# Kernel tuning notes

Measured on AMD Instinct MI355X. Metric: run time of the kernel, lower is better.

The kernel has to match this reference:

```python
import jax, jax.numpy as jnp
import numpy as np

V, D, C, B, S, H = 50000, 256, 10, 64, 512, 512


def setup_inputs() -> dict:
    key = jax.random.key(0)
    ks = jax.random.split(key, 12)
    s = 0.02
    return {
        "x": jax.random.randint(ks[0], (B, S), 0, V),
        "embed_w": jax.random.normal(ks[1], (V, D), dtype=jnp.float32) * s,
        "Wl": jax.random.normal(ks[2], (D, D), dtype=jnp.float32) * s,
        "bl": jnp.zeros((D,), jnp.float32),
        "Wsl": jax.random.normal(ks[3], (D, D), dtype=jnp.float32) * s,
        "bsl": jnp.zeros((D,), jnp.float32),
        "Wr": jax.random.normal(ks[4], (D, D), dtype=jnp.float32) * s,
        "br": jnp.zeros((D,), jnp.float32),
        "Wsr": jax.random.normal(ks[5], (D, D), dtype=jnp.float32) * s,
        "bsr": jnp.zeros((D,), jnp.float32),
        "conv_w": jax.random.normal(ks[6], (H, 3 * D), dtype=jnp.float32) * s,
        "conv_b": jnp.zeros((H,), jnp.float32),
        "fc_w": jax.random.normal(ks[7], (C, H), dtype=jnp.float32) * s,
        "fc_b": jnp.zeros((C,), jnp.float32),
        "cl0": jax.random.normal(ks[8], (B, D), dtype=jnp.float32),
        "cr0": jax.random.normal(ks[9], (B, D), dtype=jnp.float32),
    }


def reference(x, embed_w, Wl, bl, Wsl, bsl, Wr, br, Wsr, bsr,
              conv_w, conv_b, fc_w, fc_b, cl0, cr0):
    e = embed_w[x]  # [B,S,D] embedding lookup
    # Precompute the embedding-dependent half of each recurrence (one big GEMM)
    pre_l = jnp.swapaxes(jnp.einsum("bsd,ed->bse", e, Wsl) + bsl, 0, 1)  # [S,B,D]
    pre_r = jnp.swapaxes(jnp.einsum("bsd,ed->bse", e, Wsr) + bsr, 0, 1)  # [S,B,D]

    # left[0]=cl0; left[t]=relu(Wl left[t-1] + Wsl e[t-1])  (output carry, then update)
    def lstep(c, p):
        return jax.nn.relu(c @ Wl.T + bl + p), c

    _, left = jax.lax.scan(lstep, cl0, pre_l)  # [S,B,D]

    # right[S-1]=cr0; right[t]=relu(Wr right[t+1] + Wsr e[t+1])
    def rstep(c, p):
        return jax.nn.relu(c @ Wr.T + br + p), c

    _, right = jax.lax.scan(rstep, cr0, pre_r, reverse=True)  # [S,B,D]

    ctx = jnp.concatenate(
        [jnp.swapaxes(left, 0, 1), e, jnp.swapaxes(right, 0, 1)], axis=-1
    )  # [B,S,3D]
    # Conv2d(1,512,(1,3D)) == per-timestep linear 3D->512
    h = jax.nn.relu(jnp.einsum("bsd,hd->bsh", ctx, conv_w) + conv_b)  # [B,S,H]
    pooled = h.max(axis=1)  # max_pool1d over full sequence -> [B,H]
    return pooled @ fc_w.T + fc_b  # [B,C]
```

## Files before the change

### kernel.cpp

```cpp
#include <hip/hip_runtime.h>
#include <hip/hip_bf16.h>

#define VOCAB 50000
#define DD 256
#define NCLS 10
#define BB 64
#define SS 512
#define HH 512
#define K3D 768

typedef __attribute__((ext_vector_type(8))) short bf16x8;
typedef __attribute__((ext_vector_type(8))) unsigned short ush8;
typedef __attribute__((ext_vector_type(4))) float f32x4;

static __device__ __forceinline__ unsigned short f2bf(float f) {
    __hip_bfloat16 h = __float2bfloat16(f);
    return *reinterpret_cast<unsigned short*>(&h);
}

__global__ __launch_bounds__(256) void prep_gather_kernel(
    const float* __restrict__ conv_w,
    const float* __restrict__ Wsl, const float* __restrict__ Wsr,
    const float* __restrict__ bsl, const float* __restrict__ bl,
    const float* __restrict__ bsr, const float* __restrict__ br,
    const int* __restrict__ x, const float* __restrict__ embed_w,
    unsigned short* __restrict__ convwb,
    unsigned short* __restrict__ wscat,
    float* __restrict__ biascat,
    unsigned short* __restrict__ e2)
{
    const int bid = blockIdx.x;
    if (bid < 192) {
        const int g = bid * 256 + threadIdx.x;
        const float* src = conv_w + (size_t)g * 8;
        const float4 v0 = *(const float4*)(src);
        const float4 v1 = *(const float4*)(src + 4);
        ush8 o;
        o[0]=f2bf(v0.x); o[1]=f2bf(v0.y); o[2]=f2bf(v0.z); o[3]=f2bf(v0.w);
        o[4]=f2bf(v1.x); o[5]=f2bf(v1.y); o[6]=f2bf(v1.z); o[7]=f2bf(v1.w);
        *(ush8*)(convwb + (size_t)g * 8) = o;
    } else if (bid < 256) {
        const int g = (bid - 192) * 256 + threadIdx.x;
        const int row = g >> 5, d0 = (g & 31) * 8;
        const float* src = (row < 256 ? Wsl + (size_t)row * DD
                                      : Wsr + (size_t)(row - 256) * DD) + d0;
        const float4 v0 = *(const float4*)(src);
        const float4 v1 = *(const float4*)(src + 4);
        ush8 o;
        o[0]=f2bf(v0.x); o[1]=f2bf(v0.y); o[2]=f2bf(v0.z); o[3]=f2bf(v0.w);
        o[4]=f2bf(v1.x); o[5]=f2bf(v1.y); o[6]=f2bf(v1.z); o[7]=f2bf(v1.w);
        *(ush8*)(wscat + (size_t)g * 8) = o;
    } else if (bid == 256) {
        for (int i = threadIdx.x; i < 512; i += 256)
            biascat[i] = (i < 256) ? (bsl[i] + bl[i]) : (bsr[i - 256] + br[i - 256]);
    } else {
        const int g = (bid - 257) * 256 + threadIdx.x;
        const int bs = g >> 5;
        const int b = bs >> 9, s = bs & (SS - 1);
        const int d0 = (g & 31) * 8;
        const float* src = embed_w + (size_t)x[bs] * DD + d0;
        const float4 v0 = *(const float4*)(src);
        const float4 v1 = *(const float4*)(src + 4);
        ush8 o;
        o[0]=f2bf(v0.x); o[1]=f2bf(v0.y); o[2]=f2bf(v0.z); o[3]=f2bf(v0.w);
        o[4]=f2bf(v1.x); o[5]=f2bf(v1.y); o[6]=f2bf(v1.z); o[7]=f2bf(v1.w);
        *(ush8*)(e2 + ((size_t)s * BB + b) * DD + d0) = o;
    }
}

#define PPAD 72

__global__ __launch_bounds__(256) void pre_mfma_kernel(
    const unsigned short* __restrict__ wscat,
    const unsigned short* __restrict__ e2,
    const float* __restrict__ biascat,
    float* __restrict__ pre2_l, float* __restrict__ pre2_r)
{
    __shared__ unsigned short Abuf[2][128][PPAD];
    __shared__ unsigned short Bbuf[2][128][PPAD];

    const int mi  = blockIdx.x & 3;
    const int sbi = blockIdx.x >> 2;
    const int tid = threadIdx.x;
    const int w = tid >> 6, lane = tid & 63;
    const int lr = lane & 15, g = lane >> 4;
    const int lk = g * 8;

    f32x4 acc[2][8];
#pragma unroll
    for (int mt = 0; mt < 2; ++mt)
#pragma unroll
        for (int nt = 0; nt < 8; ++nt) acc[mt][nt] = (f32x4)(0.f);

    const int strow = tid >> 3;
    const int skc   = (tid & 7) * 8;

    auto stage = [&](int ks, int buf) {
        const int k0 = ks * 64;
#pragma unroll
        for (int j = 0; j < 4; ++j) {
            const int row = strow + 32 * j;
            *(bf16x8*)&Abuf[buf][row][skc] =
                *(const bf16x8*)(wscat + (size_t)(mi * 128 + row) * DD + k0 + skc);
            *(bf16x8*)&Bbuf[buf][row][skc] =
                *(const bf16x8*)(e2 + (size_t)(sbi * 128 + row) * DD + k0 + skc);
        }
    };

    stage(0, 0);
    int cur = 0;
    for (int ks = 0; ks < 4; ++ks) {
        __syncthreads();
        if (ks + 1 < 4) stage(ks + 1, cur ^ 1);
#pragma unroll
        for (int k2 = 0; k2 < 2; ++k2) {
            const int kk = k2 * 32 + lk;
            const bf16x8 a0 = *(const bf16x8*)&Abuf[cur][w * 32 + lr][kk];
            const bf16x8 a1 = *(const bf16x8*)&Abuf[cur][w * 32 + 16 + lr][kk];
#pragma unroll
            for (int nt = 0; nt < 8; ++nt) {
                const bf16x8 bv = *(const bf16x8*)&Bbuf[cur][nt * 16 + lr][kk];
                acc[0][nt] = __builtin_amdgcn_mfma_f32_16x16x32_bf16(a0, bv, acc[0][nt], 0, 0, 0);
                acc[1][nt] = __builtin_amdgcn_mfma_f32_16x16x32_bf16(a1, bv, acc[1][nt], 0, 0, 0);
            }
        }
        cur ^= 1;
    }

#pragma unroll
    for (int mt = 0; mt < 2; ++mt) {
        const int eg = mi * 128 + w * 32 + mt * 16 + g * 4;
        const float4 bia = *(const float4*)(biascat + eg);
        float* dstb = (eg >= 256) ? pre2_r : pre2_l;
        const int e = eg & 255;
#pragma unroll
        for (int nt = 0; nt < 8; ++nt) {
            const int sb = sbi * 128 + nt * 16 + lr;
            const int s = sb >> 6, bgq = (sb >> 4) & 3, b_loc = sb & 15;
            float4 v;
            v.x = acc[mt][nt][0] + bia.x;
            v.y = acc[mt][nt][1] + bia.y;
            v.z = acc[mt][nt][2] + bia.z;
            v.w = acc[mt][nt][3] + bia.w;
            *(float4*)(dstb + ((size_t)s * 4 + bgq) * 4096 + (e >> 2) * 64 + b_loc * 4) = v;
        }
    }
}

#define CSWZ(row, off) ((off) ^ (((row) & 15) << 4))
#define APAD 72

__global__ __launch_bounds__(256, 1) void recur_conve_kernel(
    const float* __restrict__ Wl, const float* __restrict__ Wr,
    const float* __restrict__ cl0, const float* __restrict__ cr0,
    const float* __restrict__ pre2_l, const float* __restrict__ pre2_r,
    unsigned short* __restrict__ outl, unsigned short* __restrict__ outr,
    const unsigned short* __restrict__ e2,
    const unsigned short* __restrict__ convwb,
    unsigned short* __restrict__ hpart)
{
    __shared__ alignas(16) unsigned char smem[2 * 2 * 128 * APAD * 2];

    const int tid  = threadIdx.x;
    const int lane = tid & 63;

    if (blockIdx.x < 8) {
        unsigned short* cbf0 = (unsigned short*)smem;
        unsigned short* cbf1 = (unsigned short*)smem + 16 * 256;

        const int dir = blockIdx.x >> 2;
        const int bg  = blockIdx.x & 3;
        const int b0  = bg * 16;
        const int wl  = tid >> 6;
        const int col = lane & 15;
        const int g   = lane >> 4;

        const float* W   = dir ? Wr : Wl;
        const float* c0  = dir ? cr0 : cl0;
        const float* pre = dir ? pre2_r : pre2_l;
        unsigned short* out = dir ? outr : outl;

        bf16x8 wfrag[4][8];
#pragma unroll
        for (int mt = 0; mt < 4; ++mt)
#pragma unroll
            for (int i = 0; i < 8; ++i) {
                const int kt = (i + 2 * wl) & 7;
                const float* src = W + (size_t)(wl * 64 + mt * 16 + col) * DD
                                     + kt * 32 + g * 8;
                const float4 lo = *(const float4*)(src);
                const float4 hi = *(const float4*)(src + 4);
                ush8 p;
                p[0]=f2bf(lo.x); p[1]=f2bf(lo.y); p[2]=f2bf(lo.z); p[3]=f2bf(lo.w);
                p[4]=f2bf(hi.x); p[5]=f2bf(hi.y); p[6]=f2bf(hi.z); p[7]=f2bf(hi.w);
                wfrag[mt][i] = *(bf16x8*)&p;
            }

        int soff[8];
#pragma unroll
        for (int i = 0; i < 8; ++i) {
            const int kt = (i + 2 * wl) & 7;
            soff[i] = CSWZ(col, kt * 64 + g * 16);
        }

        {
            const int blc = tid >> 4;
            const int ch  = tid & 15;
            const float* src = c0 + (size_t)(b0 + blc) * DD + ch * 16;
            const float4 v0 = *(const float4*)(src);
            const float4 v1 = *(const float4*)(src + 4);
            const float4 v2 = *(const float4*)(src + 8);
            const float4 v3 = *(const float4*)(src + 12);
            ush8 p0, p1;
            p0[0]=f2bf(v0.x); p0[1]=f2bf(v0.y); p0[2]=f2bf(v0.z); p0[3]=f2bf(v0.w);
            p0[4]=f2bf(v1.x); p0[5]=f2bf(v1.y); p0[6]=f2bf(v1.z); p0[7]=f2bf(v1.w);
            p1[0]=f2bf(v2.x); p1[1]=f2bf(v2.y); p1[2]=f2bf(v2.z); p1[3]=f2bf(v2.w);
            p1[4]=f2bf(v3.x); p1[5]=f2bf(v3.y); p1[6]=f2bf(v3.z); p1[7]=f2bf(v3.w);
            char* rowp = (char*)cbf0 + blc * 512;
            *(ush8*)(rowp + CSWZ(blc, ch * 32))      = p0;
            *(ush8*)(rowp + CSWZ(blc, ch * 32 + 16)) = p1;
            const int t0 = dir ? 511 : 0;
            ush8* dst = (ush8*)(out + ((size_t)t0 * BB + b0 + blc) * DD + ch * 16);
            dst[0] = p0; dst[1] = p1;
        }

        const int lpre = (wl * 16 + g) * 64 + col * 4;
        const ptrdiff_t pstep = dir ? -(ptrdiff_t)16384 : (ptrdiff_t)16384;
        const float* p0 = pre + ((size_t)(dir ? 511 : 0) * 4 + bg) * 4096 + lpre;

        float4 pA0 = *(const float4*)(p0);
        float4 pA1 = *(const float4*)(p0 + 256);
        float4 pA2 = *(const float4*)(p0 + 512);
        float4 pA3 = *(const float4*)(p0 + 768);
        const float* p1p = p0 + pstep;
        float4 pB0 = *(const float4*)(p1p);
        float4 pB1 = *(const float4*)(p1p + 256);
        float4 pB2 = *(const float4*)(p1p + 512);
        float4 pB3 = *(const float4*)(p1p + 768);
        const float* pfetch = p0 + 2 * pstep;

        unsigned short* oplane = out + (size_t)(dir ? 510 : 1) * BB * DD
                                     + (b0 + col) * DD + wl * 64 + g * 4;
        const ptrdiff_t ostep = (dir ? -(ptrdiff_t)1 : (ptrdiff_t)1) * (BB * DD);

        __syncthreads();

        int cur = 0;
#pragma unroll 2
        for (int k = 0; k < SS - 1; ++k) {
            bf16x8 sfrag[8];
            {
                const char* rowp = (const char*)(cur ? cbf1 : cbf0) + col * 512;
#pragma unroll
                for (int i = 0; i < 8; ++i)
                    sfrag[i] = *(const bf16x8*)(rowp + soff[i]);
            }

            const float4 pN0 = *(const float4*)(pfetch);
            const float4 pN1 = *(const float4*)(pfetch + 256);
            const float4 pN2 = *(const float4*)(pfetch + 512);
            const float4 pN3 = *(const float4*)(pfetch + 768);
            if (k < SS - 4) pfetch += pstep;

            char* nbuf = (char*)(cur ? cbf0 : cbf1) + col * 512;

            auto epi = [&](int mt, const f32x4 a) {
                const float v0 = fmaxf(a[0], 0.f);
                const float v1 = fmaxf(a[1], 0.f);
                const float v2 = fmaxf(a[2], 0.f);
                const float v3 = fmaxf(a[3], 0.f);
                uint2 uu;
                asm("v_cvt_pk_bf16_f32 %0, %1, %2" : "=v"(uu.x) : "v"(v0), "v"(v1));
                asm("v_cvt_pk_bf16_f32 %0, %1, %2" : "=v"(uu.y) : "v"(v2), "v"(v3));
                const int eoff = (wl * 64 + mt * 16 + g * 4) * 2;
                *(uint2*)(nbuf + CSWZ(col, eoff)) = uu;
                *(uint2*)(oplane + mt * 16) = uu;
            };

            f32x4 a0 = *(const f32x4*)&pA0;
            f32x4 a1 = *(const f32x4*)&pA1;
            __builtin_amdgcn_s_setprio(1);
#pragma unroll
            for (int i = 0; i < 8; ++i) {
                a0 = __builtin_amdgcn_mfma_f32_16x16x32_bf16(wfrag[0][i], sfrag[i], a0, 0, 0, 0);
                a1 = __builtin_amdgcn_mfma_f32_16x16x32_bf16(wfrag[1][i], sfrag[i], a1, 0, 0, 0);
            }
            __builtin_amdgcn_s_setprio(0);
            epi(0, a0);
            epi(1, a1);

            f32x4 a2 = *(const f32x4*)&pA2;
            f32x4 a3 = *(const f32x4*)&pA3;
            __builtin_amdgcn_s_setprio(1);
#pragma unroll
            for (int i = 0; i < 8; ++i) {
                a2 = __builtin_amdgcn_mfma_f32_16x16x32_bf16(wfrag[2][i], sfrag[i], a2, 0, 0, 0);
                a3 = __builtin_amdgcn_mfma_f32_16x16x32_bf16(wfrag[3][i], sfrag[i], a3, 0, 0, 0);
            }
            __builtin_amdgcn_s_setprio(0);
            epi(2, a2);
            epi(3, a3);

            pA0 = pB0; pA1 = pB1; pA2 = pB2; pA3 = pB3;
            pB0 = pN0; pB1 = pN1; pB2 = pN2; pB3 = pN3;
            oplane += ostep;

            asm volatile("s_waitcnt lgkmcnt(0)" ::: "memory");
            __builtin_amdgcn_s_barrier();
            asm volatile("" ::: "memory");
            cur ^= 1;
        }
        return;
    }

    unsigned short* Ab = (unsigned short*)smem;
    unsigned short* Bb = (unsigned short*)smem + 2 * 128 * APAD;

    const int wid = tid >> 6;
    const int lr  = lane & 15;
    const int lk  = (lane >> 4) * 8;
    const int strow = tid >> 3;
    const int skc   = (tid & 7) * 8;

    for (int rep = 0; rep < 2; ++rep) {
        const int cid = (blockIdx.x - 8) + rep * 128;
        const int b   = cid >> 2;
        const int h0  = (cid & 3) * 128;

        f32x4 acc[2][8];
#pragma unroll
        for (int st = 0; st < 2; ++st)
#pragma unroll
            for (int ht = 0; ht < 8; ++ht) acc[st][ht] = (f32x4)(0.f);

        auto stage = [&](int it, int buf) {
            const int stile = it >> 2, kstep = it & 3;
            const int k0 = kstep * 64;
            const int s0 = stile * 128;
#pragma unroll
            for (int j = 0; j < 4; ++j) {
                const int row = strow + 32 * j;
                const int ss = s0 + row;
                *(bf16x8*)&Ab[(buf * 128 + row) * APAD + skc] =
                    *(const bf16x8*)(e2 + ((size_t)ss * BB + b) * DD + k0 + skc);
                *(bf16x8*)&Bb[(buf * 128 + row) * APAD + skc] =
                    *(const bf16x8*)(convwb + (size_t)(h0 + row) * K3D + 256 + k0 + skc);
            }
        };

        stage(0, 0);
        int cur = 0;
        for (int it = 0; it < 16; ++it) {
            __syncthreads();
            if (it + 1 < 16) stage(it + 1, cur ^ 1);

            const int wrow0 = wid * 32;
#pragma unroll
            for (int ks = 0; ks < 2; ++ks) {
                const int kk = ks * 32 + lk;
                const bf16x8 a0 = *(const bf16x8*)&Ab[(cur * 128 + wrow0 + lr) * APAD + kk];
                const bf16x8 a1 = *(const bf16x8*)&Ab[(cur * 128 + wrow0 + 16 + lr) * APAD + kk];
#pragma unroll
                for (int ht = 0; ht < 8; ++ht) {
                    const bf16x8 bv = *(const bf16x8*)&Bb[(cur * 128 + ht * 16 + lr) * APAD + kk];
                    acc[0][ht] = __builtin_amdgcn_mfma_f32_16x16x32_bf16(a0, bv, acc[0][ht], 0, 0, 0);
                    acc[1][ht] = __builtin_amdgcn_mfma_f32_16x16x32_bf16(a1, bv, acc[1][ht], 0, 0, 0);
                }
            }
            if ((it & 3) == 3) {
                const int stile = it >> 2;
                unsigned short* hp = hpart + (size_t)(cid * 4 + stile) * 16384;
#pragma unroll
                for (int st = 0; st < 2; ++st)
#pragma unroll
                    for (int ht = 0; ht < 8; ++ht) {
                        uint2 uu;
                        asm("v_cvt_pk_bf16_f32 %0, %1, %2"
                            : "=v"(uu.x) : "v"(acc[st][ht][0]), "v"(acc[st][ht][1]));
                        asm("v_cvt_pk_bf16_f32 %0, %1, %2"
                            : "=v"(uu.y) : "v"(acc[st][ht][2]), "v"(acc[st][ht][3]));
                        const int f = (wid * 2 + st) * 8 + ht;
                        *(uint2*)(hp + f * 256 + lane * 4) = uu;
                        acc[st][ht] = (f32x4)(0.f);
                    }
            }
            cur ^= 1;
        }
        __syncthreads();
    }
}

#define KSTEP 64
#define NKC 8
#define NST 4

__global__ __launch_bounds__(256) void conv_pool_kernel(
    const unsigned short* __restrict__ leftb,
    const unsigned short* __restrict__ rightb,
    const unsigned short* __restrict__ convwb,
    const unsigned short* __restrict__ hpart,
    const float* __restrict__ conv_b,
    float* __restrict__ pooled)
{
    __shared__ unsigned short Abuf[2][128][APAD];
    __shared__ unsigned short Bbuf[2][128][APAD];
    __shared__ float red[4][128];

    const int b   = blockIdx.x >> 2;
    const int h0  = (blockIdx.x & 3) * 128;
    const int tid = threadIdx.x;
    const int wid = tid >> 6;
    const int lane = tid & 63;
    const int lr  = lane & 15;
    const int lk  = (lane >> 4) * 8;

    float pmax[8];
#pragma unroll
    for (int ht = 0; ht < 8; ++ht) pmax[ht] = -INFINITY;

    const int strow = tid >> 3;
    const int skc   = (tid & 7) * 8;

    auto stage = [&](int it, int buf) {
        const int stile = it / NKC, kstep = it % NKC;
        const int k0 = kstep * KSTEP;
        const int s0 = stile * 128;
        const unsigned short* asrc;
        int koff, bcol;
        if (k0 < DD) { asrc = leftb;  koff = k0;      bcol = k0; }
        else         { asrc = rightb; koff = k0 - DD; bcol = k0 + 256; }
#pragma unroll
        for (int j = 0; j < 4; ++j) {
            const int row = strow + 32 * j;
            const int ss = s0 + row;
            *(bf16x8*)&Abuf[buf][row][skc] =
                *(const bf16x8*)(asrc + ((size_t)ss * BB + b) * DD + koff + skc);
            *(bf16x8*)&Bbuf[buf][row][skc] =
                *(const bf16x8*)(convwb + (size_t)(h0 + row) * K3D + bcol + skc);
        }
    };

    f32x4 acc[2][8];
    auto load_hinit = [&](int stile) {
        const unsigned short* hp = hpart + (size_t)(blockIdx.x * 4 + stile) * 16384;
#pragma unroll
        for (int st = 0; st < 2; ++st)
#pragma unroll
            for (int ht = 0; ht < 8; ++ht) {
                const int f = (wid * 2 + st) * 8 + ht;
                const uint2 uu = *(const uint2*)(hp + f * 256 + lane * 4);
                f32x4 v;
                v[0] = __uint_as_float(uu.x << 16);
                v[1] = __uint_as_float(uu.x & 0xffff0000u);
                v[2] = __uint_as_float(uu.y << 16);
                v[3] = __uint_as_float(uu.y & 0xffff0000u);
                acc[st][ht] = v;
            }
    };

    load_hinit(0);
    stage(0, 0);
    int cur = 0;
    for (int it = 0; it < NST * NKC; ++it) {
        __syncthreads();
        if (it + 1 < NST * NKC) stage(it + 1, cur ^ 1);

        const int wrow0 = wid * 32;
#pragma unroll
        for (int ks = 0; ks < 2; ++ks) {
            const int kk = ks * 32 + lk;
            const bf16x8 a0 = *(const bf16x8*)&Abuf[cur][wrow0 + lr][kk];
            const bf16x8 a1 = *(const bf16x8*)&Abuf[cur][wrow0 + 16 + lr][kk];
#pragma unroll
            for (int ht = 0; ht < 8; ++ht) {
                const bf16x8 bv = *(const bf16x8*)&Bbuf[cur][ht * 16 + lr][kk];
                acc[0][ht] = __builtin_amdgcn_mfma_f32_16x16x32_bf16(a0, bv, acc[0][ht], 0, 0, 0);
                acc[1][ht] = __builtin_amdgcn_mfma_f32_16x16x32_bf16(a1, bv, acc[1][ht], 0, 0, 0);
            }
        }
        if ((it % NKC) == NKC - 1) {
#pragma unroll
            for (int st = 0; st < 2; ++st)
#pragma unroll
                for (int ht = 0; ht < 8; ++ht)
#pragma unroll
                    for (int r = 0; r < 4; ++r)
                        pmax[ht] = fmaxf(pmax[ht], acc[st][ht][r]);
            if (it + 1 < NST * NKC) load_hinit((it + 1) / NKC);
        }
        cur ^= 1;
    }

#pragma unroll
    for (int ht = 0; ht < 8; ++ht) {
        float m = pmax[ht];
        m = fmaxf(m, __shfl_xor(m, 16));
        m = fmaxf(m, __shfl_xor(m, 32));
        if (lane < 16) red[wid][ht * 16 + lane] = m;
    }
    __syncthreads();
    if (tid < 128) {
        const float m = fmaxf(fmaxf(red[0][tid], red[1][tid]),
                              fmaxf(red[2][tid], red[3][tid]));
        pooled[(size_t)b * HH + h0 + tid] = fmaxf(m + conv_b[h0 + tid], 0.f);
    }
}

__global__ void fc_kernel(const float* __restrict__ pooled,
                          const float* __restrict__ fc_w,
                          const float* __restrict__ fc_b,
                          float* __restrict__ out)
{
    const int t = threadIdx.x;
    if (t >= BB * NCLS) return;
    const int b = t / NCLS, c = t % NCLS;
    float acc = fc_b[c];
    for (int h = 0; h < HH; ++h)
        acc += pooled[(size_t)b * HH + h] * fc_w[(size_t)c * HH + h];
    out[b * NCLS + c] = acc;
}

extern "C" void kernel_launch(void* const* d_in, const int* in_sizes, int n_in,
                              void* d_out, int out_size, void* d_ws, size_t ws_size,
                              hipStream_t stream)
{
    const int*   x       = (const int*)  d_in[0];
    const float* embed_w = (const float*)d_in[1];
    const float* Wl      = (const float*)d_in[2];
    const float* bl      = (const float*)d_in[3];
    const float* Wsl     = (const float*)d_in[4];
    const float* bsl     = (const float*)d_in[5];
    const float* Wr      = (const float*)d_in[6];
    const float* br      = (const float*)d_in[7];
    const float* Wsr     = (const float*)d_in[8];
    const float* bsr     = (const float*)d_in[9];
    const float* conv_w  = (const float*)d_in[10];
    const float* conv_b  = (const float*)d_in[11];
    const float* fc_w    = (const float*)d_in[12];
    const float* fc_b    = (const float*)d_in[13];
    const float* cl0     = (const float*)d_in[14];
    const float* cr0     = (const float*)d_in[15];
    float* out = (float*)d_out;

    char* ws = (char*)d_ws;
    const size_t SZf = (size_t)SS * BB * DD * sizeof(float);
    const size_t SZh = (size_t)SS * BB * DD * sizeof(unsigned short);
    float*          pre2_l = (float*)(ws);
    float*          pre2_r = (float*)(ws + SZf);
    unsigned short* leftb  = (unsigned short*)(ws + 2 * SZf);
    unsigned short* rightb = (unsigned short*)(ws + 2 * SZf + SZh);
    unsigned short* e2     = (unsigned short*)(ws + 2 * SZf + 2 * SZh);
    unsigned short* convwb = (unsigned short*)(ws + 2 * SZf + 3 * SZh);
    unsigned short* wscat  = (unsigned short*)(ws + 2 * SZf + 3 * SZh + (size_t)HH * K3D * 2);
    float*          biascat= (float*)(ws + 2 * SZf + 3 * SZh + (size_t)HH * K3D * 2 + (size_t)512 * DD * 2);
    float*          pooled = (float*)(ws + 2 * SZf + 3 * SZh + (size_t)HH * K3D * 2 + (size_t)512 * DD * 2 + 2048);
    unsigned short* hpart  = (unsigned short*)(ws + 2 * SZf + 3 * SZh + (size_t)HH * K3D * 2 + (size_t)512 * DD * 2 + 2048 + (size_t)BB * HH * 4);

    prep_gather_kernel<<<257 + (BB * SS * DD / 8) / 256, 256, 0, stream>>>(
        conv_w, Wsl, Wsr, bsl, bl, bsr, br, x, embed_w,
        convwb, wscat, biascat, e2);

    pre_mfma_kernel<<<1024, 256, 0, stream>>>(wscat, e2, biascat, pre2_l, pre2_r);

    recur_conve_kernel<<<136, 256, 0, stream>>>(
        Wl, Wr, cl0, cr0, pre2_l, pre2_r, leftb, rightb, e2, convwb, hpart);

    conv_pool_kernel<<<BB * (HH / 128), 256, 0, stream>>>(
        leftb, rightb, convwb, hpart, conv_b, pooled);

    fc_kernel<<<1, BB * NCLS, 0, stream>>>(pooled, fc_w, fc_b, out);
}
```

Baseline: 447.0 us.

## Fuse prep gather into pre-GEMM and split conv pooling across sequence tiles

Merges the conversion/gather kernel with the pre-activation GEMM. The GEMM blocks now gather embedding rows and Ws weights straight from fp32 and convert them in the staging step, which removes one launch and the wscat/biascat round trip. The conv-pool kernel is split four ways along the sequence, giving 1024 blocks instead of 256, and each block folds its partial max into pooled with atomicMax on float bits after a memset. That is valid because the post-ReLU values are non-negative. The cost is redundant embedding gathers across the four M-blocks, an extra memset launch and atomic traffic.

Result: faster. 437.7 us (-2.1%).

```diff
diff --git a/kernel.cpp b/kernel.cpp
--- a/kernel.cpp
+++ b/kernel.cpp
@@ -18,132 +18,118 @@
     return *reinterpret_cast<unsigned short*>(&h);
 }
 
-__global__ __launch_bounds__(256) void prep_gather_kernel(
-    const float* __restrict__ conv_w,
+static __device__ __forceinline__ ush8 cvt8(const float* src) {
+    const float4 lo = *(const float4*)(src);
+    const float4 hi = *(const float4*)(src + 4);
+    ush8 o;
+    o[0]=f2bf(lo.x); o[1]=f2bf(lo.y); o[2]=f2bf(lo.z); o[3]=f2bf(lo.w);
+    o[4]=f2bf(hi.x); o[5]=f2bf(hi.y); o[6]=f2bf(hi.z); o[7]=f2bf(hi.w);
+    return o;
+}
+
+#define PPAD 72
+
+__global__ __launch_bounds__(256) void prep_pre_kernel(
     const float* __restrict__ Wsl, const float* __restrict__ Wsr,
     const float* __restrict__ bsl, const float* __restrict__ bl,
     const float* __restrict__ bsr, const float* __restrict__ br,
     const int* __restrict__ x, const float* __restrict__ embed_w,
+    const float* __restrict__ conv_w,
     unsigned short* __restrict__ convwb,
-    unsigned short* __restrict__ wscat,
-    float* __restrict__ biascat,
-    unsigned short* __restrict__ e2)
-{
-    const int bid = blockIdx.x;
-    if (bid < 192) {
-        const int g = bid * 256 + threadIdx.x;
-        const float* src = conv_w + (size_t)g * 8;
-        const float4 v0 = *(const float4*)(src);
-        const float4 v1 = *(const float4*)(src + 4);
-        ush8 o;
-        o[0]=f2bf(v0.x); o[1]=f2bf(v0.y); o[2]=f2bf(v0.z); o[3]=f2bf(v0.w);
-        o[4]=f2bf(v1.x); o[5]=f2bf(v1.y); o[6]=f2bf(v1.z); o[7]=f2bf(v1.w);
-        *(ush8*)(convwb + (size_t)g * 8) = o;
-    } else if (bid < 256) {
-        const int g = (bid - 192) * 256 + threadIdx.x;
-        const int row = g >> 5, d0 = (g & 31) * 8;
-        const float* src = (row < 256 ? Wsl + (size_t)row * DD
-                                      : Wsr + (size_t)(row - 256) * DD) + d0;
-        const float4 v0 = *(const float4*)(src);
-        const float4 v1 = *(const float4*)(src + 4);
-        ush8 o;
-        o[0]=f2bf(v0.x); o[1]=f2bf(v0.y); o[2]=f2bf(v0.z); o[3]=f2bf(v0.w);
-        o[4]=f2bf(v1.x); o[5]=f2bf(v1.y); o[6]=f2bf(v1.z); o[7]=f2bf(v1.w);
-        *(ush8*)(wscat + (size_t)g * 8) = o;
-    } else if (bid == 256) {
-        for (int i = threadIdx.x; i < 512; i += 256)
-            biascat[i] = (i < 256) ? (bsl[i] + bl[i]) : (bsr[i - 256] + br[i - 256]);
-    } else {
-        const int g = (bid - 257) * 256 + threadIdx.x;
-        const int bs = g >> 5;
-        const int b = bs >> 9, s = bs & (SS - 1);
-        const int d0 = (g & 31) * 8;
-        const float* src = embed_w + (size_t)x[bs] * DD + d0;
-        const float4 v0 = *(const float4*)(src);
-        const float4 v1 = *(const float4*)(src + 4);
-        ush8 o;
-        o[0]=f2bf(v0.x); o[1]=f2bf(v0.y); o[2]=f2bf(v0.z); o[3]=f2bf(v0.w);
-        o[4]=f2bf(v1.x); o[5]=f2bf(v1.y); o[6]=f2bf(v1.z); o[7]=f2bf(v1.w);
-        *(ush8*)(e2 + ((size_t)s * BB + b) * DD + d0) = o;
-    }
-}
-
-#define PPAD 72
-
-__global__ __launch_bounds__(256) void pre_mfma_kernel(
-    const unsigned short* __restrict__ wscat,
-    const unsigned short* __restrict__ e2,
-    const float* __restrict__ biascat,
+    unsigned short* __restrict__ e2,
     float* __restrict__ pre2_l, float* __restrict__ pre2_r)
 {
     __shared__ unsigned short Abuf[2][128][PPAD];
     __shared__ unsigned short Bbuf[2][128][PPAD];
-
-    const int mi  = blockIdx.x & 3;
-    const int sbi = blockIdx.x >> 2;
+    __shared__ int xs[128];
+
+    const int bid = blockIdx.x;
     const int tid = threadIdx.x;
-    const int w = tid >> 6, lane = tid & 63;
-    const int lr = lane & 15, g = lane >> 4;
-    const int lk = g * 8;
-
-    f32x4 acc[2][8];
-#pragma unroll
-    for (int mt = 0; mt < 2; ++mt)
-#pragma unroll
-        for (int nt = 0; nt < 8; ++nt) acc[mt][nt] = (f32x4)(0.f);
-
-    const int strow = tid >> 3;
-    const int skc   = (tid & 7) * 8;
-
-    auto stage = [&](int ks, int buf) {
-        const int k0 = ks * 64;
-#pragma unroll
-        for (int j = 0; j < 4; ++j) {
-            const int row = strow + 32 * j;
-            *(bf16x8*)&Abuf[buf][row][skc] =
-                *(const bf16x8*)(wscat + (size_t)(mi * 128 + row) * DD + k0 + skc);
-            *(bf16x8*)&Bbuf[buf][row][skc] =
-                *(const bf16x8*)(e2 + (size_t)(sbi * 128 + row) * DD + k0 + skc);
-        }
-    };
-
-    stage(0, 0);
-    int cur = 0;
-    for (int ks = 0; ks < 4; ++ks) {
+
+    if (bid < 1024) {
+        const int mi  = bid & 3;
+        const int sbi = bid >> 2;
+        const int w = tid >> 6, lane = tid & 63;
+        const int lr = lane & 15, g = lane >> 4;
+        const int lk = g * 8;
+        const int strow = tid >> 3;
+        const int skc   = (tid & 7) * 8;
+
+        if (tid < 128)
+            xs[tid] = x[(tid & 63) * SS + 2 * sbi + (tid >> 6)];
+
+        f32x4 acc[2][8];
+#pragma unroll
+        for (int mt = 0; mt < 2; ++mt)
+#pragma unroll
+            for (int nt = 0; nt < 8; ++nt) acc[mt][nt] = (f32x4)(0.f);
+
+        auto stage = [&](int ks, int buf) {
+            const int k0 = ks * 64;
+#pragma unroll
+            for (int j = 0; j < 4; ++j) {
+                const int row = strow + 32 * j;
+                const float* wsrc = (mi < 2 ? Wsl + (size_t)(mi * 128 + row) * DD
+                                            : Wsr + (size_t)((mi - 2) * 128 + row) * DD)
+                                    + k0 + skc;
+                *(ush8*)&Abuf[buf][row][skc] = cvt8(wsrc);
+                const float* esrc = embed_w + (size_t)xs[row] * DD + k0 + skc;
+                *(ush8*)&Bbuf[buf][row][skc] = cvt8(esrc);
+            }
+        };
+
         __syncthreads();
-        if (ks + 1 < 4) stage(ks + 1, cur ^ 1);
-#pragma unroll
-        for (int k2 = 0; k2 < 2; ++k2) {
-            const int kk = k2 * 32 + lk;
-            const bf16x8 a0 = *(const bf16x8*)&Abuf[cur][w * 32 + lr][kk];
-            const bf16x8 a1 = *(const bf16x8*)&Abuf[cur][w * 32 + 16 + lr][kk];
+        stage(0, 0);
+        int cur = 0;
+        for (int ks = 0; ks < 4; ++ks) {
+            __syncthreads();
+            if (ks + 1 < 4) stage(ks + 1, cur ^ 1);
+#pragma unroll
+            for (int k2 = 0; k2 < 2; ++k2) {
+                const int kk = k2 * 32 + lk;
+                const bf16x8 a0 = *(const bf16x8*)&Abuf[cur][w * 32 + lr][kk];
+                const bf16x8 a1 = *(const bf16x8*)&Abuf[cur][w * 32 + 16 + lr][kk];
+#pragma unroll
+                for (int nt = 0; nt < 8; ++nt) {
+                    const bf16x8 bv = *(const bf16x8*)&Bbuf[cur][nt * 16 + lr][kk];
+                    acc[0][nt] = __builtin_amdgcn_mfma_f32_16x16x32_bf16(a0, bv, acc[0][nt], 0, 0, 0);
+                    acc[1][nt] = __builtin_amdgcn_mfma_f32_16x16x32_bf16(a1, bv, acc[1][nt], 0, 0, 0);
+                }
+            }
+            cur ^= 1;
+        }
+
+#pragma unroll
+        for (int mt = 0; mt < 2; ++mt) {
+            const int eg = mi * 128 + w * 32 + mt * 16 + g * 4;
+            const int e  = eg & 255;
+            const float* bsx = (eg < 256) ? bsl : bsr;
+            const float* bbx = (eg < 256) ? bl  : br;
+            const float4 b1 = *(const float4*)(bsx + e);
+            const float4 b2 = *(const float4*)(bbx + e);
+            float* dstb = (eg >= 256) ? pre2_r : pre2_l;
 #pragma unroll
             for (int nt = 0; nt < 8; ++nt) {
-                const bf16x8 bv = *(const bf16x8*)&Bbuf[cur][nt * 16 + lr][kk];
-                acc[0][nt] = __builtin_amdgcn_mfma_f32_16x16x32_bf16(a0, bv, acc[0][nt], 0, 0, 0);
-                acc[1][nt] = __builtin_amdgcn_mfma_f32_16x16x32_bf16(a1, bv, acc[1][nt], 0, 0, 0);
-            }
-        }
-        cur ^= 1;
-    }
-
-#pragma unroll
-    for (int mt = 0; mt < 2; ++mt) {
-        const int eg = mi * 128 + w * 32 + mt * 16 + g * 4;
-        const float4 bia = *(const float4*)(biascat + eg);
-        float* dstb = (eg >= 256) ? pre2_r : pre2_l;
-        const int e = eg & 255;
-#pragma unroll
-        for (int nt = 0; nt < 8; ++nt) {
-            const int sb = sbi * 128 + nt * 16 + lr;
-            const int s = sb >> 6, bgq = (sb >> 4) & 3, b_loc = sb & 15;
-            float4 v;
-            v.x = acc[mt][nt][0] + bia.x;
-            v.y = acc[mt][nt][1] + bia.y;
-            v.z = acc[mt][nt][2] + bia.z;
-            v.w = acc[mt][nt][3] + bia.w;
-            *(float4*)(dstb + ((size_t)s * 4 + bgq) * 4096 + (e >> 2) * 64 + b_loc * 4) = v;
-        }
+                const int sb = sbi * 128 + nt * 16 + lr;
+                const int s = sb >> 6, bgq = (sb >> 4) & 3, b_loc = sb & 15;
+                float4 v;
+                v.x = acc[mt][nt][0] + b1.x + b2.x;
+                v.y = acc[mt][nt][1] + b1.y + b2.y;
+                v.z = acc[mt][nt][2] + b1.z + b2.z;
+                v.w = acc[mt][nt][3] + b1.w + b2.w;
+                *(float4*)(dstb + ((size_t)s * 4 + bgq) * 4096 + (e >> 2) * 64 + b_loc * 4) = v;
+            }
+        }
+    } else if (bid < 1216) {
+        const int g = (bid - 1024) * 256 + tid;
+        *(ush8*)(convwb + (size_t)g * 8) = cvt8(conv_w + (size_t)g * 8);
+    } else {
+        const int g = (bid - 1216) * 256 + tid;
+        const int bs = g >> 5;
+        const int b = bs >> 9, s = bs & (SS - 1);
+        const int d0 = (g & 31) * 8;
+        *(ush8*)(e2 + ((size_t)s * BB + b) * DD + d0) =
+            cvt8(embed_w + (size_t)x[bs] * DD + d0);
     }
 }
 
@@ -188,11 +174,7 @@
                 const int kt = (i + 2 * wl) & 7;
                 const float* src = W + (size_t)(wl * 64 + mt * 16 + col) * DD
                                      + kt * 32 + g * 8;
-                const float4 lo = *(const float4*)(src);
-                const float4 hi = *(const float4*)(src + 4);
-                ush8 p;
-                p[0]=f2bf(lo.x); p[1]=f2bf(lo.y); p[2]=f2bf(lo.z); p[3]=f2bf(lo.w);
-                p[4]=f2bf(hi.x); p[5]=f2bf(hi.y); p[6]=f2bf(hi.z); p[7]=f2bf(hi.w);
+                const ush8 p = cvt8(src);
                 wfrag[mt][i] = *(bf16x8*)&p;
             }
 
@@ -207,15 +189,8 @@
             const int blc = tid >> 4;
             const int ch  = tid & 15;
             const float* src = c0 + (size_t)(b0 + blc) * DD + ch * 16;
-            const float4 v0 = *(const float4*)(src);
-            const float4 v1 = *(const float4*)(src + 4);
-            const float4 v2 = *(const float4*)(src + 8);
-            const float4 v3 = *(const float4*)(src + 12);
-            ush8 p0, p1;
-            p0[0]=f2bf(v0.x); p0[1]=f2bf(v0.y); p0[2]=f2bf(v0.z); p0[3]=f2bf(v0.w);
-            p0[4]=f2bf(v1.x); p0[5]=f2bf(v1.y); p0[6]=f2bf(v1.z); p0[7]=f2bf(v1.w);
-            p1[0]=f2bf(v2.x); p1[1]=f2bf(v2.y); p1[2]=f2bf(v2.z); p1[3]=f2bf(v2.w);
-            p1[4]=f2bf(v3.x); p1[5]=f2bf(v3.y); p1[6]=f2bf(v3.z); p1[7]=f2bf(v3.w);
+            const ush8 p0 = cvt8(src);
+            const ush8 p1 = cvt8(src + 8);
             char* rowp = (char*)cbf0 + blc * 512;
             *(ush8*)(rowp + CSWZ(blc, ch * 32))      = p0;
             *(ush8*)(rowp + CSWZ(blc, ch * 32 + 16)) = p1;
@@ -392,7 +367,6 @@
 
 #define KSTEP 64
 #define NKC 8
-#define NST 4
 
 __global__ __launch_bounds__(256) void conv_pool_kernel(
     const unsigned short* __restrict__ leftb,
@@ -406,43 +380,23 @@
     __shared__ unsigned short Bbuf[2][128][APAD];
     __shared__ float red[4][128];
 
-    const int b   = blockIdx.x >> 2;
-    const int h0  = (blockIdx.x & 3) * 128;
+    const int stile = blockIdx.x & 3;
+    const int h0i   = (blockIdx.x >> 2) & 3;
+    const int b     = blockIdx.x >> 4;
+    const int h0    = h0i * 128;
+    const int s0    = stile * 128;
     const int tid = threadIdx.x;
     const int wid = tid >> 6;
     const int lane = tid & 63;
     const int lr  = lane & 15;
     const int lk  = (lane >> 4) * 8;
-
-    float pmax[8];
-#pragma unroll
-    for (int ht = 0; ht < 8; ++ht) pmax[ht] = -INFINITY;
-
     const int strow = tid >> 3;
     const int skc   = (tid & 7) * 8;
 
-    auto stage = [&](int it, int buf) {
-        const int stile = it / NKC, kstep = it % NKC;
-        const int k0 = kstep * KSTEP;
-        const int s0 = stile * 128;
-        const unsigned short* asrc;
-        int koff, bcol;
-        if (k0 < DD) { asrc = leftb;  koff = k0;      bcol = k0; }
-        else         { asrc = rightb; koff = k0 - DD; bcol = k0 + 256; }
-#pragma unroll
-        for (int j = 0; j < 4; ++j) {
-            const int row = strow + 32 * j;
-            const int ss = s0 + row;
-            *(bf16x8*)&Abuf[buf][row][skc] =
-                *(const bf16x8*)(asrc + ((size_t)ss * BB + b) * DD + koff + skc);
-            *(bf16x8*)&Bbuf[buf][row][skc] =
-                *(const bf16x8*)(convwb + (size_t)(h0 + row) * K3D + bcol + skc);
-        }
-    };
-
     f32x4 acc[2][8];
-    auto load_hinit = [&](int stile) {
-        const unsigned short* hp = hpart + (size_t)(blockIdx.x * 4 + stile) * 16384;
+    {
+        const unsigned short* hp = hpart
+            + ((size_t)((b * 4 + h0i) * 4 + stile)) * 16384;
 #pragma unroll
         for (int st = 0; st < 2; ++st)
 #pragma unroll
@@ -456,14 +410,30 @@
                 v[3] = __uint_as_float(uu.y & 0xffff0000u);
                 acc[st][ht] = v;
             }
+    }
+
+    auto stage = [&](int kstep, int buf) {
+        const int k0 = kstep * KSTEP;
+        const unsigned short* asrc;
+        int koff, bcol;
+        if (k0 < DD) { asrc = leftb;  koff = k0;      bcol = k0; }
+        else         { asrc = rightb; koff = k0 - DD; bcol = k0 + 256; }
+#pragma unroll
+        for (int j = 0; j < 4; ++j) {
+            const int row = strow + 32 * j;
+            const int ss = s0 + row;
+            *(bf16x8*)&Abuf[buf][row][skc] =
+                *(const bf16x8*)(asrc + ((size_t)ss * BB + b) * DD + koff + skc);
+            *(bf16x8*)&Bbuf[buf][row][skc] =
+                *(const bf16x8*)(convwb + (size_t)(h0 + row) * K3D + bcol + skc);
+        }
     };
 
-    load_hinit(0);
     stage(0, 0);
     int cur = 0;
-    for (int it = 0; it < NST * NKC; ++it) {
+    for (int it = 0; it < NKC; ++it) {
         __syncthreads();
-        if (it + 1 < NST * NKC) stage(it + 1, cur ^ 1);
+        if (it + 1 < NKC) stage(it + 1, cur ^ 1);
 
         const int wrow0 = wid * 32;
 #pragma unroll
@@ -478,22 +448,18 @@
                 acc[1][ht] = __builtin_amdgcn_mfma_f32_16x16x32_bf16(a1, bv, acc[1][ht], 0, 0, 0);
             }
         }
-        if ((it % NKC) == NKC - 1) {
-#pragma unroll
-            for (int st = 0; st < 2; ++st)
-#pragma unroll
-                for (int ht = 0; ht < 8; ++ht)
-#pragma unroll
-                    for (int r = 0; r < 4; ++r)
-                        pmax[ht] = fmaxf(pmax[ht], acc[st][ht][r]);
-            if (it + 1 < NST * NKC) load_hinit((it + 1) / NKC);
-        }
         cur ^= 1;
     }
 
+    float pmax[8];
 #pragma unroll
     for (int ht = 0; ht < 8; ++ht) {
-        float m = pmax[ht];
+        float m = -INFINITY;
+#pragma unroll
+        for (int st = 0; st < 2; ++st)
+#pragma unroll
+            for (int r = 0; r < 4; ++r)
+                m = fmaxf(m, acc[st][ht][r]);
         m = fmaxf(m, __shfl_xor(m, 16));
         m = fmaxf(m, __shfl_xor(m, 32));
         if (lane < 16) red[wid][ht * 16 + lane] = m;
@@ -502,7 +468,9 @@
     if (tid < 128) {
         const float m = fmaxf(fmaxf(red[0][tid], red[1][tid]),
                               fmaxf(red[2][tid], red[3][tid]));
-        pooled[(size_t)b * HH + h0 + tid] = fmaxf(m + conv_b[h0 + tid], 0.f);
+        const float v = fmaxf(m + conv_b[h0 + tid], 0.f);
+        atomicMax((unsigned*)(pooled + (size_t)b * HH + h0 + tid),
+                  __float_as_uint(v));
     }
 }
 
@@ -551,21 +519,21 @@
     unsigned short* rightb = (unsigned short*)(ws + 2 * SZf + SZh);
     unsigned short* e2     = (unsigned short*)(ws + 2 * SZf + 2 * SZh);
     unsigned short* convwb = (unsigned short*)(ws + 2 * SZf + 3 * SZh);
-    unsigned short* wscat  = (unsigned short*)(ws + 2 * SZf + 3 * SZh + (size_t)HH * K3D * 2);
-    float*          biascat= (float*)(ws + 2 * SZf + 3 * SZh + (size_t)HH * K3D * 2 + (size_t)512 * DD * 2);
-    float*          pooled = (float*)(ws + 2 * SZf + 3 * SZh + (size_t)HH * K3D * 2 + (size_t)512 * DD * 2 + 2048);
-    unsigned short* hpart  = (unsigned short*)(ws + 2 * SZf + 3 * SZh + (size_t)HH * K3D * 2 + (size_t)512 * DD * 2 + 2048 + (size_t)BB * HH * 4);
-
-    prep_gather_kernel<<<257 + (BB * SS * DD / 8) / 256, 256, 0, stream>>>(
-        conv_w, Wsl, Wsr, bsl, bl, bsr, br, x, embed_w,
-        convwb, wscat, biascat, e2);
-
-    pre_mfma_kernel<<<1024, 256, 0, stream>>>(wscat, e2, biascat, pre2_l, pre2_r);
+    float*          pooled = (float*)(ws + 2 * SZf + 3 * SZh + (size_t)HH * K3D * 2);
+    unsigned short* hpart  = (unsigned short*)(ws + 2 * SZf + 3 * SZh
+                                               + (size_t)HH * K3D * 2
+                                               + (size_t)BB * HH * 4);
+
+    hipMemsetAsync(pooled, 0, (size_t)BB * HH * sizeof(float), stream);
+
+    prep_pre_kernel<<<5312, 256, 0, stream>>>(
+        Wsl, Wsr, bsl, bl, bsr, br, x, embed_w, conv_w,
+        convwb, e2, pre2_l, pre2_r);
 
     recur_conve_kernel<<<136, 256, 0, stream>>>(
         Wl, Wr, cl0, cr0, pre2_l, pre2_r, leftb, rightb, e2, convwb, hpart);
 
-    conv_pool_kernel<<<BB * (HH / 128), 256, 0, stream>>>(
+    conv_pool_kernel<<<1024, 256, 0, stream>>>(
         leftb, rightb, convwb, hpart, conv_b, pooled);
 
     fc_kernel<<<1, BB * NCLS, 0, stream>>>(pooled, fc_w, fc_b, out);
```
